# Optimization experiments

Hardware: AMD Instinct MI355X
Metric: run time of the kernel (lower is better)

Reference implementation:

```python
import jax, jax.numpy as jnp
import numpy as np

N, E, M, H, D, G, C = 50000, 400000, 4, 400, 3, 128, 10
BN_EPS = 1e-5


def setup_inputs() -> dict:
    key = jax.random.key(0)
    ks = iter(jax.random.split(key, 64))

    def rn(shape, s=0.05):
        return (jax.random.normal(next(ks), shape, jnp.float32) * s)

    inp = {}
    inp['x'] = jax.random.normal(next(ks), (N, M), jnp.float32)
    inp['edge_index'] = jax.random.randint(next(ks), (2, E), 0, N, dtype=jnp.int32)
    inp['batch'] = jnp.sort(jax.random.randint(next(ks), (N,), 0, G, dtype=jnp.int32))
    inp['num_graphs'] = G
    # first GINConv MLP: M -> H -> H -> H
    inp['c0_w1'] = rn((H, M)); inp['c0_b1'] = rn((H,))
    inp['c0_g1'] = jnp.ones((H,), jnp.float32); inp['c0_be1'] = jnp.zeros((H,), jnp.float32)
    inp['c0_w2'] = rn((H, H)); inp['c0_b2'] = rn((H,))
    inp['c0_g2'] = jnp.ones((H,), jnp.float32); inp['c0_be2'] = jnp.zeros((H,), jnp.float32)
    inp['c0_w3'] = rn((H, H)); inp['c0_b3'] = rn((H,))
    # GINConv layers 1..D-1 (stacked): H -> H -> H -> H
    L = D - 1
    inp['cw1'] = rn((L, H, H)); inp['cb1'] = rn((L, H))
    inp['cg1'] = jnp.ones((L, H), jnp.float32); inp['cbe1'] = jnp.zeros((L, H), jnp.float32)
    inp['cw2'] = rn((L, H, H)); inp['cb2'] = rn((L, H))
    inp['cg2'] = jnp.ones((L, H), jnp.float32); inp['cbe2'] = jnp.zeros((L, H), jnp.float32)
    inp['cw3'] = rn((L, H, H)); inp['cb3'] = rn((L, H))
    # readout head
    inp['lin1_w'] = rn((H * D // 2, H * D)); inp['lin1_b'] = rn((H * D // 2,))
    inp['lin2_w'] = rn((C, H * D // 2)); inp['lin2_b'] = rn((C,))
    return inp


def _bn(z, g, b):
    # training-mode BatchNorm1d over nodes (biased variance, eps=1e-5)
    m = z.mean(axis=0)
    v = ((z - m) ** 2).mean(axis=0)
    return (z - m) * jax.lax.rsqrt(v + BN_EPS) * g + b


def _mlp(h, w1, b1, g1, be1, w2, b2, g2, be2, w3, b3):
    # PyG MLP(num_layers=3): Lin->BN->ReLU, Lin->BN->ReLU, Lin (plain last)
    h = jax.nn.relu(_bn(h @ w1.T + b1, g1, be1))
    h = jax.nn.relu(_bn(h @ w2.T + b2, g2, be2))
    return h @ w3.T + b3


def reference(x, edge_index, batch, num_graphs,
              c0_w1, c0_b1, c0_g1, c0_be1, c0_w2, c0_b2, c0_g2, c0_be2, c0_w3, c0_b3,
              cw1, cb1, cg1, cbe1, cw2, cb2, cg2, cbe2, cw3, cb3,
              lin1_w, lin1_b, lin2_w, lin2_b):
    src, dst = edge_index[0], edge_index[1]
    n = x.shape[0]

    def gin_agg(h):
        # eps = -1.0 => (1+eps)*x_i term vanishes; pure neighbor scatter-add
        return jax.ops.segment_sum(h[src], dst, num_segments=n)

    pools = []
    h = _mlp(gin_agg(x), c0_w1, c0_b1, c0_g1, c0_be1,
             c0_w2, c0_b2, c0_g2, c0_be2, c0_w3, c0_b3)
    pools.append(jax.ops.segment_sum(h, batch, num_segments=num_graphs))
    for i in range(D - 1):
        h = _mlp(gin_agg(h), cw1[i], cb1[i], cg1[i], cbe1[i],
                 cw2[i], cb2[i], cg2[i], cbe2[i], cw3[i], cb3[i])
        pools.append(jax.ops.segment_sum(h, batch, num_segments=num_graphs))
    xG = jnp.concatenate(pools, axis=1)                 # [G, D*H]
    z = jax.nn.relu(xG @ lin1_w.T + lin1_b)             # dropout off (eval)
    z = z @ lin2_w.T + lin2_b
    return jax.nn.log_softmax(z, axis=1)
```

## Files before the change

kernel.cpp:

```cpp
#include <hip/hip_runtime.h>
#include <hip/hip_bf16.h>
#include <math.h>
#include <cstdint>

static constexpr int NN = 50000;
static constexpr int NE = 400000;
static constexpr int H  = 400;
static constexpr int NG = 128;
static constexpr int NC = 10;
static constexpr float EPS = 1e-5f;
static constexpr int NB1 = (NN + 255) / 256;
static constexpr int KP  = 416;
static constexpr int SREP = 8;
static constexpr int SSLOT = SREP * 2 * KP;

typedef unsigned short u16;
typedef __attribute__((ext_vector_type(8))) unsigned short u16x8;
typedef __attribute__((ext_vector_type(4))) unsigned short u16x4;
typedef __attribute__((ext_vector_type(8))) short bf16x8;
typedef __attribute__((ext_vector_type(4))) float f32x4;

__device__ __forceinline__ float bf2f(u16 u) {
    return __uint_as_float(((uint32_t)u) << 16);
}
__device__ __forceinline__ u16 f2bf(float f) {
    uint32_t u = __float_as_uint(f);
    return (u16)((u + 0x7FFFu + ((u >> 16) & 1u)) >> 16);
}
__device__ __forceinline__ void gload_lds16(const void* g, void* lds) {
    __builtin_amdgcn_global_load_lds((const __attribute__((address_space(1))) void*)g,
                                     (__attribute__((address_space(3))) void*)lds, 16, 0, 0);
}

__device__ __forceinline__ bf16x8 bnrelu8(bf16x8 a, const float* __restrict__ scp,
                                          const float* __restrict__ shp) {
    union { bf16x8 v; uint32_t u[4]; } in, out;
    in.v = a;
#pragma unroll
    for (int p = 0; p < 4; ++p) {
        float lo = __uint_as_float(in.u[p] << 16);
        float hi = __uint_as_float(in.u[p] & 0xFFFF0000u);
        lo = fmaxf(fmaf(lo, scp[2 * p], shp[2 * p]), 0.f);
        hi = fmaxf(fmaf(hi, scp[2 * p + 1], shp[2 * p + 1]), 0.f);
        asm("v_cvt_pk_bf16_f32 %0, %1, %2" : "=v"(out.u[p]) : "v"(lo), "v"(hi));
    }
    return out.v;
}


__global__ void k_count(const int* __restrict__ dst, int* __restrict__ deg) {
    int e = blockIdx.x * blockDim.x + threadIdx.x;
    if (e < NE) atomicAdd(&deg[dst[e]], 1);
}

__global__ __launch_bounds__(256) void k_scan1(const int* __restrict__ deg,
                                               int* __restrict__ part,
                                               int* __restrict__ btot) {
    __shared__ int sd[256];
    int t = threadIdx.x;
    int i = blockIdx.x * 256 + t;
    int v = (i < NN) ? deg[i] : 0;
    sd[t] = v;
    __syncthreads();
#pragma unroll
    for (int off = 1; off < 256; off <<= 1) {
        int x = (t >= off) ? sd[t - off] : 0;
        __syncthreads();
        sd[t] += x;
        __syncthreads();
    }
    if (i < NN) part[i] = sd[t];
    if (t == 255) btot[blockIdx.x] = sd[255];
}

__global__ __launch_bounds__(256) void k_scan2(int* __restrict__ btot) {
    __shared__ int sd[256];
    int t = threadIdx.x;
    int v = (t < NB1) ? btot[t] : 0;
    sd[t] = v;
    __syncthreads();
#pragma unroll
    for (int off = 1; off < 256; off <<= 1) {
        int x = (t >= off) ? sd[t - off] : 0;
        __syncthreads();
        sd[t] += x;
        __syncthreads();
    }
    if (t < NB1) btot[t] = sd[t];
}

__global__ __launch_bounds__(256) void k_scan3(const int* __restrict__ part,
                                               const int* __restrict__ btot,
                                               const int* __restrict__ deg,
                                               int* __restrict__ rowp,
                                               int* __restrict__ cur,
                                               const int* __restrict__ batch,
                                               int* __restrict__ cnt) {
    __shared__ int hh[NG];
    int t = threadIdx.x;
    int i = blockIdx.x * 256 + t;
    if (i < NN) {
        int s = part[i] + (blockIdx.x ? btot[blockIdx.x - 1] : 0);
        rowp[i + 1] = s;
        cur[i] = s - deg[i];
    }
    if (i == 0) rowp[0] = 0;
    for (int j = t; j < NG; j += 256) hh[j] = 0;
    __syncthreads();
    if (i < NN) atomicAdd(&hh[batch[i]], 1);
    __syncthreads();
    for (int j = t; j < NG; j += 256)
        if (hh[j]) atomicAdd(&cnt[j], hh[j]);
}

__global__ void k_scatter(const int* __restrict__ src, const int* __restrict__ dst,
                          int* __restrict__ cur, int* __restrict__ csrc) {
    int e = blockIdx.x * blockDim.x + threadIdx.x;
    if (e < NE) {
        int d = dst[e];
        int p = atomicAdd(&cur[d], 1);
        csrc[p] = src[e];
    }
}


__global__ __launch_bounds__(256) void k_wprep(const float* __restrict__ c0_w2,
                                               const float* __restrict__ cw2,
                                               const float* __restrict__ cw1,
                                               const float* __restrict__ c0_w3,
                                               const float* __restrict__ cw3,
                                               const float* __restrict__ c0_b3,
                                               const float* __restrict__ cb3,
                                               u16* __restrict__ wpad,
                                               float* __restrict__ bb1,
                                               float* __restrict__ bb2) {
    const int b = blockIdx.x;
    const int t = threadIdx.x;
    if (b < 244) {
        int i = b * 256 + t;
        if (i >= 3 * 400 * 52) return;
        int rc = i / 52;
        int c8 = (i % 52) * 8;
        u16x8 o = {0, 0, 0, 0, 0, 0, 0, 0};
        if (c8 < 400) {
            int mat = rc / 400, row = rc % 400;
            const float* s = (mat == 0 ? c0_w2 : mat == 1 ? cw2 : cw2 + 160000)
                             + (long)row * 400;
            float4 a = *(const float4*)(s + c8);
            float4 bb = *(const float4*)(s + c8 + 4);
            o[0] = f2bf(a.x); o[1] = f2bf(a.y); o[2] = f2bf(a.z); o[3] = f2bf(a.w);
            o[4] = f2bf(bb.x); o[5] = f2bf(bb.y); o[6] = f2bf(bb.z); o[7] = f2bf(bb.w);
        }
        *(u16x8*)(wpad + (long)rc * KP + c8) = o;
    } else if (b < 342) {
        __shared__ float As[16][68];
        __shared__ float Bs[16][68];
        const int b2 = (b < 293) ? b - 244 : b - 293;
        const float* Wa = (b < 293) ? cw1 : cw1 + 160000;
        const float* Wb = (b < 293) ? c0_w3 : cw3;
        u16* dst = wpad + (size_t)((b < 293) ? 3 : 4) * 400 * KP;
        const int bc = (b2 / 7) * 64, bj = (b2 % 7) * 64;
        const int tx = t & 15, ty = t >> 4;
        float acc[4][4] = {};
        for (int k0 = 0; k0 < 400; k0 += 16) {
            {
                int c = bc + (t >> 2);
                int kq = (t & 3) * 4;
                float4 v = make_float4(0.f, 0.f, 0.f, 0.f);
                if (c < 400) v = *(const float4*)(Wa + (long)c * 400 + k0 + kq);
                As[kq + 0][t >> 2] = v.x; As[kq + 1][t >> 2] = v.y;
                As[kq + 2][t >> 2] = v.z; As[kq + 3][t >> 2] = v.w;
            }
            {
                int k = k0 + (t >> 4);
                int jq = (t & 15) * 4;
                int j = bj + jq;
                float4 v = make_float4(0.f, 0.f, 0.f, 0.f);
                if (j < 400) v = *(const float4*)(Wb + (long)k * 400 + j);
                Bs[t >> 4][jq + 0] = v.x; Bs[t >> 4][jq + 1] = v.y;
                Bs[t >> 4][jq + 2] = v.z; Bs[t >> 4][jq + 3] = v.w;
            }
            __syncthreads();
#pragma unroll
            for (int kk = 0; kk < 16; ++kk) {
                float4 av = *(const float4*)&As[kk][ty * 4];
                float4 bv = *(const float4*)&Bs[kk][tx * 4];
                float a[4] = {av.x, av.y, av.z, av.w};
                float bb[4] = {bv.x, bv.y, bv.z, bv.w};
#pragma unroll
                for (int i = 0; i < 4; ++i)
#pragma unroll
                    for (int j = 0; j < 4; ++j)
                        acc[i][j] = fmaf(a[i], bb[j], acc[i][j]);
            }
            __syncthreads();
        }
#pragma unroll
        for (int i = 0; i < 4; ++i) {
            int c = bc + ty * 4 + i;
            if (c >= 400) continue;
#pragma unroll
            for (int j = 0; j < 4; ++j) {
                int col = bj + tx * 4 + j;
                if (col < KP) dst[(long)c * KP + col] = (col < 400) ? f2bf(acc[i][j]) : 0;
            }
        }
    } else {
        const int c = (b & 1) * 256 + t;
        if (c >= 400) return;
        const float* Wa = (b < 344) ? cw1 : cw1 + 160000;
        const float* bv = (b < 344) ? c0_b3 : cb3;
        float* out = (b < 344) ? bb1 : bb2;
        const float4* wr = (const float4*)(Wa + (long)c * 400);
        const float4* br = (const float4*)bv;
        float s0 = 0.f, s1 = 0.f, s2 = 0.f, s3 = 0.f;
        for (int q = 0; q < 100; ++q) {
            float4 a = wr[q], v = br[q];
            s0 = fmaf(a.x, v.x, s0); s1 = fmaf(a.y, v.y, s1);
            s2 = fmaf(a.z, v.z, s2); s3 = fmaf(a.w, v.w, s3);
        }
        out[c] = s0 + s1 + s2 + s3;
    }
}


__global__ __launch_bounds__(256) void k_agg0(const float* __restrict__ x,
                                              const int* __restrict__ rowp,
                                              const int* __restrict__ csrc,
                                              float* __restrict__ out,
                                              float* __restrict__ mom) {
    __shared__ float ws[4][14];
    int n = blockIdx.x * blockDim.x + threadIdx.x;
    float4 acc = make_float4(0.f, 0.f, 0.f, 0.f);
    if (n < NN) {
        int b = rowp[n], e = rowp[n + 1];
        for (int p = b; p < e; ++p) {
            float4 v = ((const float4*)x)[csrc[p]];
            acc.x += v.x; acc.y += v.y; acc.z += v.z; acc.w += v.w;
        }
        ((float4*)out)[n] = acc;
    }
    float mv[14] = {acc.x, acc.y, acc.z, acc.w,
                    acc.x * acc.x, acc.x * acc.y, acc.x * acc.z, acc.x * acc.w,
                    acc.y * acc.y, acc.y * acc.z, acc.y * acc.w,
                    acc.z * acc.z, acc.z * acc.w, acc.w * acc.w};
    int wv = threadIdx.x >> 6, l = threadIdx.x & 63;
#pragma unroll
    for (int i = 0; i < 14; ++i) {
        float s = mv[i];
#pragma unroll
        for (int o = 32; o; o >>= 1) s += __shfl_xor(s, o);
        if (l == 0) ws[wv][i] = s;
    }
    __syncthreads();
    if (threadIdx.x < 14) {
        float s = ws[0][threadIdx.x] + ws[1][threadIdx.x] + ws[2][threadIdx.x] + ws[3][threadIdx.x];
        atomicAdd(&mom[threadIdx.x], s);
    }
}


__global__ __launch_bounds__(256) void k_aggH(const u16* __restrict__ h,
                                              const int* __restrict__ rowp,
                                              const int* __restrict__ csrc,
                                              const float* __restrict__ bias,
                                              u16* __restrict__ out) {
    int n = (blockIdx.x << 2) + (threadIdx.x >> 6);
    if (n >= NN) return;
    int l = threadIdx.x & 63;
    if (l >= 50) return;
    float4 b0 = *(const float4*)(bias + l * 8);
    float4 b1 = *(const float4*)(bias + l * 8 + 4);
    float acc[8] = {b0.x, b0.y, b0.z, b0.w, b1.x, b1.y, b1.z, b1.w};
    int b = rowp[n], e = rowp[n + 1];
    for (int p = b; p < e; ++p) {
        const u16* r = h + (long)csrc[p] * H + l * 8;
        u16x8 v = *(const u16x8*)r;
#pragma unroll
        for (int q = 0; q < 8; ++q) acc[q] += bf2f(v[q]);
    }
    u16x8 o;
#pragma unroll
    for (int q = 0; q < 8; ++q) o[q] = f2bf(acc[q]);
    *(u16x8*)(out + (long)n * H + l * 8) = o;
}


static constexpr int NLIN0 = (int)(((long)NN * 100 + 255) / 256);

__global__ void k_lin0(const float* __restrict__ a4, const float* __restrict__ w,
                       const float* __restrict__ b, u16* __restrict__ out,
                       const float* __restrict__ mom, float* __restrict__ slot0) {
    if (blockIdx.x >= NLIN0) {
        int j = (blockIdx.x - NLIN0) * 256 + threadIdx.x;
        if (j >= 400) return;
        float4 wv = ((const float4*)w)[j];
        float dot = wv.x * mom[0] + wv.y * mom[1] + wv.z * mom[2] + wv.w * mom[3];
        float quad = wv.x * wv.x * mom[4] + 2.f * wv.x * wv.y * mom[5]
                   + 2.f * wv.x * wv.z * mom[6] + 2.f * wv.x * wv.w * mom[7]
                   + wv.y * wv.y * mom[8] + 2.f * wv.y * wv.z * mom[9]
                   + 2.f * wv.y * wv.w * mom[10] + wv.z * wv.z * mom[11]
                   + 2.f * wv.z * wv.w * mom[12] + wv.w * wv.w * mom[13];
        float bj = b[j];
        slot0[j] = dot + (float)NN * bj;
        slot0[KP + j] = quad + 2.f * bj * dot + (float)NN * bj * bj;
        return;
    }
    long i = (long)blockIdx.x * blockDim.x + threadIdx.x;
    if (i >= (long)NN * 100) return;
    int n = (int)(i / 100), q = (int)(i - (long)n * 100);
    int j0 = q * 4;
    float4 av = ((const float4*)a4)[n];
    u16x4 o;
#pragma unroll
    for (int jj = 0; jj < 4; ++jj) {
        float4 wv = ((const float4*)w)[j0 + jj];
        float s = fmaf(av.x, wv.x, fmaf(av.y, wv.y, fmaf(av.z, wv.z, av.w * wv.w)));
        o[jj] = f2bf(s + b[j0 + jj]);
    }
    *(u16x4*)(out + (long)n * H + j0) = o;
}


__global__ __launch_bounds__(256) void k_statsv(const u16* __restrict__ z,
                                                float* __restrict__ stats) {
    __shared__ float ls[800];
    int t = threadIdx.x;
    for (int i = t; i < 800; i += 256) ls[i] = 0.f;
    __syncthreads();
    if (t < 250) {
        int sub = t / 50, seg = t % 50;
        float s[8] = {0, 0, 0, 0, 0, 0, 0, 0};
        float q[8] = {0, 0, 0, 0, 0, 0, 0, 0};
        for (int r = blockIdx.x * 5 + sub; r < NN; r += gridDim.x * 5) {
            u16x8 v = *(const u16x8*)(z + (long)r * H + seg * 8);
#pragma unroll
            for (int j = 0; j < 8; ++j) {
                float f = bf2f(v[j]);
                s[j] += f; q[j] += f * f;
            }
        }
#pragma unroll
        for (int j = 0; j < 8; ++j) {
            atomicAdd(&ls[seg * 8 + j], s[j]);
            atomicAdd(&ls[400 + seg * 8 + j], q[j]);
        }
    }
    __syncthreads();
    const int rep = blockIdx.x & (SREP - 1);
    for (int i = t; i < 800; i += 256) {
        int col = (i < 400) ? i : (i - 400 + KP);
        atomicAdd(&stats[rep * 2 * KP + col], ls[i]);
    }
}


template <bool STATS>
__global__ __launch_bounds__(256) void gemm_mfma(const u16* __restrict__ A,
                                                 const u16* __restrict__ Wp,
                                                 const float* __restrict__ bias,
                                                 const float* __restrict__ bnG,
                                                 const float* __restrict__ bnBe,
                                                 const float* __restrict__ statsIn,
                                                 float* __restrict__ statsOut,
                                                 u16* __restrict__ out, int M) {
    constexpr int BUF = 6656;
    __shared__ u16 lds[3 * BUF];
    __shared__ float sdScale[KP];
    __shared__ float sdShift[KP];
    __shared__ float sst[160];

    const int t = threadIdx.x;
    const int nwg = gridDim.x;
    const int q8 = nwg >> 3, r8 = nwg & 7;
    const int xcd = blockIdx.x & 7, jj = blockIdx.x >> 3;
    const int wgid = (xcd < r8 ? xcd * (q8 + 1) : r8 * (q8 + 1) + (xcd - r8) * q8) + jj;
    const int bm = (wgid / 5) * 128;
    const int bn = (wgid % 5) * 80;
    const int w = t >> 6, l = t & 63;

    for (int j = t; j < KP; j += 256) {
        float s = 0.f, q = 0.f;
#pragma unroll
        for (int r = 0; r < SREP; ++r) {
            s += statsIn[r * 2 * KP + j];
            q += statsIn[r * 2 * KP + KP + j];
        }
        float sc = 0.f, sh = 0.f;
        if (j < H) {
            float m = s / NN;
            float v = fmaxf(q / NN - m * m, 0.f);
            float rs = rsqrtf(v + EPS);
            sc = bnG[j] * rs;
            sh = bnBe[j] - m * sc;
        }
        sdScale[j] = sc;
        sdShift[j] = sh;
    }

    const int srow = l >> 2;
    const int sck  = ((l & 3) ^ ((l >> 3) & 3)) * 8;

    auto stageTile = [&](int b, int kt) {
        u16* dst = lds + b * BUF;
        const int k0 = kt * 32;
        long g0 = (long)bm + w * 16 + srow;
        long g1 = g0 + 64;
        if (g0 > M - 1) g0 = M - 1;
        if (g1 > M - 1) g1 = M - 1;
        gload_lds16(A + g0 * 400 + k0 + sck, dst + w * 512);
        gload_lds16(A + g1 * 400 + k0 + sck, dst + (w + 4) * 512);
        gload_lds16(Wp + (long)(bn + w * 16 + srow) * KP + k0 + sck,
                    dst + 4096 + w * 512);
        gload_lds16(Wp + (long)(bn + 64 + srow) * KP + k0 + sck,
                    dst + 4096 + 4 * 512);
    };

    f32x4 acc[2][5];
#pragma unroll
    for (int i = 0; i < 2; ++i)
#pragma unroll
        for (int c = 0; c < 5; ++c)
            acc[i][c] = (f32x4){0.f, 0.f, 0.f, 0.f};

    const int r16 = l & 15;
    const int cc  = l >> 4;
    const int swz = r16 * 32 + (((cc ^ ((r16 >> 1) & 3))) << 3);

    auto computeTile = [&](int b, int s) {
        const u16* base = lds + b * BUF;
        const u16* ab = base + w * 1024 + swz;
        const u16* bb = base + 4096 + swz;
        bf16x8 fa0 = *(const bf16x8*)ab;
        bf16x8 fa1 = *(const bf16x8*)(ab + 512);
        const int k = s * 32 + cc * 8;
        fa0 = bnrelu8(fa0, sdScale + k, sdShift + k);
        fa1 = bnrelu8(fa1, sdScale + k, sdShift + k);
        __builtin_amdgcn_s_setprio(1);
#pragma unroll
        for (int c = 0; c < 5; ++c) {
            bf16x8 fb = *(const bf16x8*)(bb + c * 512);
            acc[0][c] = __builtin_amdgcn_mfma_f32_16x16x32_bf16(fa0, fb, acc[0][c], 0, 0, 0);
            acc[1][c] = __builtin_amdgcn_mfma_f32_16x16x32_bf16(fa1, fb, acc[1][c], 0, 0, 0);
        }
        __builtin_amdgcn_s_setprio(0);
    };

    stageTile(0, 0);
    stageTile(1, 1);

#pragma unroll 1
    for (int s = 0; s < 12; ++s) {
        asm volatile("s_waitcnt vmcnt(4)" ::: "memory");
        __builtin_amdgcn_s_barrier();
        if (s + 2 < 13) stageTile((s + 2) % 3, s + 2);
        computeTile(s % 3, s);
    }
    asm volatile("s_waitcnt vmcnt(0)" ::: "memory");
    __builtin_amdgcn_s_barrier();
    computeTile(12 % 3, 12);

    u16* tile = lds;
    __syncthreads();
    if (STATS) for (int i = t; i < 160; i += 256) sst[i] = 0.f;
    if (STATS) __syncthreads();

    float ssum[5], sqq[5];
#pragma unroll
    for (int c = 0; c < 5; ++c) { ssum[c] = 0.f; sqq[c] = 0.f; }
#pragma unroll
    for (int i = 0; i < 2; ++i) {
        const int lrow0 = w * 32 + i * 16 + (l >> 4) * 4;
#pragma unroll
        for (int c = 0; c < 5; ++c) {
            const int lcol = c * 16 + (l & 15);
            const float bv = bias[bn + lcol];
#pragma unroll
            for (int r = 0; r < 4; ++r) {
                const int lrow = lrow0 + r;
                float z = acc[i][c][r] + bv;
                tile[lrow * 80 + lcol] = f2bf(z);
                if (STATS && bm + lrow < M) { ssum[c] += z; sqq[c] += z * z; }
            }
        }
    }
    __syncthreads();
#pragma unroll
    for (int j = 0; j < 5; ++j) {
        int chunk = t + j * 256;
        int row = chunk / 10, c8 = chunk % 10;
        if (bm + row < M) {
            u16x8 v = *(const u16x8*)(tile + row * 80 + c8 * 8);
            *(u16x8*)(out + (long)(bm + row) * H + bn + c8 * 8) = v;
        }
    }
    if (STATS) {
        const int rep = wgid & (SREP - 1);
#pragma unroll
        for (int c = 0; c < 5; ++c) {
            ssum[c] += __shfl_xor(ssum[c], 16); ssum[c] += __shfl_xor(ssum[c], 32);
            sqq[c]  += __shfl_xor(sqq[c], 16);  sqq[c]  += __shfl_xor(sqq[c], 32);
        }
        if (l < 16) {
#pragma unroll
            for (int c = 0; c < 5; ++c) {
                atomicAdd(&sst[c * 16 + l], ssum[c]);
                atomicAdd(&sst[80 + c * 16 + l], sqq[c]);
            }
        }
        __syncthreads();
        if (t < 80)       atomicAdd(&statsOut[rep * 2 * KP + bn + t], sst[t]);
        else if (t < 160) atomicAdd(&statsOut[rep * 2 * KP + KP + bn + (t - 80)], sst[t]);
    }
}


__global__ __launch_bounds__(256) void k_poolf(const u16* __restrict__ z,
                                               const float* __restrict__ statsIn,
                                               const float* __restrict__ gw,
                                               const float* __restrict__ be,
                                               const int* __restrict__ batch,
                                               float* __restrict__ pf) {
    __shared__ float sdS[400];
    __shared__ float sdH[400];
    int t = threadIdx.x;
    for (int j = t; j < 400; j += 256) {
        float s = 0.f, q = 0.f;
#pragma unroll
        for (int r = 0; r < SREP; ++r) {
            s += statsIn[r * 2 * KP + j];
            q += statsIn[r * 2 * KP + KP + j];
        }
        float m = s / NN, v = fmaxf(q / NN - m * m, 0.f);
        float rs = rsqrtf(v + EPS);
        float sc = gw[j] * rs;
        sdS[j] = sc;
        sdH[j] = be[j] - m * sc;
    }
    __syncthreads();
    if (t >= 250) return;
    const int sub = t / 50, seg = t % 50;
    float sc[8], sh[8];
#pragma unroll
    for (int q = 0; q < 8; ++q) {
        sc[q] = sdS[seg * 8 + q];
        sh[q] = sdH[seg * 8 + q];
    }
    int rows = (NN + gridDim.x - 1) / gridDim.x;
    int r0 = blockIdx.x * rows;
    int r1 = min(r0 + rows, NN);
    float acc[8] = {0.f, 0.f, 0.f, 0.f, 0.f, 0.f, 0.f, 0.f};
    int gp = -1;
    for (int r = r0 + sub; r < r1; r += 5) {
        int gg = batch[r];
        if (gg != gp) {
            if (gp >= 0) {
#pragma unroll
                for (int q = 0; q < 8; ++q)
                    atomicAdd(&pf[(long)gp * 400 + seg * 8 + q], acc[q]);
            }
#pragma unroll
            for (int q = 0; q < 8; ++q) acc[q] = 0.f;
            gp = gg;
        }
        u16x8 v = *(const u16x8*)(z + (long)r * H + seg * 8);
#pragma unroll
        for (int q = 0; q < 8; ++q)
            acc[q] += fmaxf(fmaf(bf2f(v[q]), sc[q], sh[q]), 0.f);
    }
    if (gp >= 0) {
#pragma unroll
        for (int q = 0; q < 8; ++q)
            atomicAdd(&pf[(long)gp * 400 + seg * 8 + q], acc[q]);
    }
}


__global__ __launch_bounds__(256) void k_poolgemm(const float* __restrict__ pf,
                                                  const float* __restrict__ w30,
                                                  const float* __restrict__ w312,
                                                  const float* __restrict__ b30,
                                                  const float* __restrict__ b312,
                                                  const int* __restrict__ cnt,
                                                  float* __restrict__ pools) {
    __shared__ __align__(16) float xr[400];
    int g = blockIdx.x, L = blockIdx.y, t = threadIdx.x;
    const float* w = (L == 0) ? w30 : w312 + (size_t)(L - 1) * 400 * 400;
    const float* b = (L == 0) ? b30 : b312 + (L - 1) * 400;
    for (int i = t; i < 400; i += 256) xr[i] = pf[((long)L * NG + g) * 400 + i];
    __syncthreads();
    float cg = (float)cnt[g];
    for (int c = t; c < 400; c += 256) {
        const float4* wr = (const float4*)(w + (long)c * 400);
        const float4* xv = (const float4*)xr;
        float s0 = 0.f, s1 = 0.f, s2 = 0.f, s3 = 0.f;
        for (int q = 0; q < 100; ++q) {
            float4 a = xv[q], bb = wr[q];
            s0 = fmaf(a.x, bb.x, s0); s1 = fmaf(a.y, bb.y, s1);
            s2 = fmaf(a.z, bb.z, s2); s3 = fmaf(a.w, bb.w, s3);
        }
        pools[(long)g * 1200 + L * 400 + c] = s0 + s1 + s2 + s3 + cg * b[c];
    }
}


__global__ __launch_bounds__(256) void k_lin1(const float* __restrict__ pools,
                                              const float* __restrict__ w1,
                                              const float* __restrict__ b1,
                                              float* __restrict__ zz) {
    __shared__ __align__(16) float xg[8][1200];
    const int bandj = blockIdx.x * 40;
    const int g0 = blockIdx.y * 8;
    const int t = threadIdx.x;
    for (int i = t; i < 9600; i += 256)
        xg[i / 1200][i % 1200] = pools[(long)(g0 + i / 1200) * 1200 + (i % 1200)];
    __syncthreads();
    const int wv = t >> 6, l = t & 63;
    for (int jj = wv; jj < 40; jj += 4) {
        const int j = bandj + jj;
        const float4* wr = (const float4*)(w1 + (long)j * 1200);
        float s[8] = {0.f, 0.f, 0.f, 0.f, 0.f, 0.f, 0.f, 0.f};
        for (int q = l; q < 300; q += 64) {
            float4 wq = wr[q];
#pragma unroll
            for (int g = 0; g < 8; ++g) {
                float4 xv = *(const float4*)&xg[g][q * 4];
                s[g] = fmaf(wq.x, xv.x, s[g]);
                s[g] = fmaf(wq.y, xv.y, s[g]);
                s[g] = fmaf(wq.z, xv.z, s[g]);
                s[g] = fmaf(wq.w, xv.w, s[g]);
            }
        }
#pragma unroll
        for (int g = 0; g < 8; ++g)
#pragma unroll
            for (int o = 32; o; o >>= 1) s[g] += __shfl_xor(s[g], o);
        if (l == 0) {
            const float bj = b1[j];
#pragma unroll
            for (int g = 0; g < 8; ++g)
                zz[(long)(g0 + g) * 600 + j] = fmaxf(s[g] + bj, 0.f);
        }
    }
}

__global__ __launch_bounds__(64) void k_lin2(const float* __restrict__ zz,
                                             const float* __restrict__ w2,
                                             const float* __restrict__ b2,
                                             float* __restrict__ out) {
    int g = blockIdx.x;
    int l = threadIdx.x;
    float p[NC];
#pragma unroll
    for (int c = 0; c < NC; ++c) p[c] = 0.f;
    for (int k = l; k < 600; k += 64) {
        float zv = zz[(long)g * 600 + k];
#pragma unroll
        for (int c = 0; c < NC; ++c) p[c] = fmaf(zv, w2[c * 600 + k], p[c]);
    }
#pragma unroll
    for (int c = 0; c < NC; ++c)
#pragma unroll
        for (int o = 32; o; o >>= 1) p[c] += __shfl_xor(p[c], o);
    if (l == 0) {
        float lg[NC];
        float mx = -1e30f;
#pragma unroll
        for (int c = 0; c < NC; ++c) { lg[c] = p[c] + b2[c]; mx = fmaxf(mx, lg[c]); }
        float se = 0.f;
#pragma unroll
        for (int c = 0; c < NC; ++c) se += expf(lg[c] - mx);
        float lse = logf(se);
#pragma unroll
        for (int c = 0; c < NC; ++c) out[(long)g * NC + c] = lg[c] - mx - lse;
    }
}


extern "C" void kernel_launch(void* const* d_in, const int* in_sizes, int n_in,
                              void* d_out, int out_size, void* d_ws, size_t ws_size,
                              hipStream_t stream) {
    const float* x      = (const float*)d_in[0];
    const int*   ei     = (const int*)d_in[1];
    const int*   batch  = (const int*)d_in[2];
    const float* c0_w1  = (const float*)d_in[4];
    const float* c0_b1  = (const float*)d_in[5];
    const float* c0_g1  = (const float*)d_in[6];
    const float* c0_be1 = (const float*)d_in[7];
    const float* c0_w2  = (const float*)d_in[8];
    const float* c0_b2  = (const float*)d_in[9];
    const float* c0_g2  = (const float*)d_in[10];
    const float* c0_be2 = (const float*)d_in[11];
    const float* c0_w3  = (const float*)d_in[12];
    const float* c0_b3  = (const float*)d_in[13];
    const float* cw1    = (const float*)d_in[14];
    const float* cb1    = (const float*)d_in[15];
    const float* cg1    = (const float*)d_in[16];
    const float* cbe1   = (const float*)d_in[17];
    const float* cw2    = (const float*)d_in[18];
    const float* cb2    = (const float*)d_in[19];
    const float* cg2    = (const float*)d_in[20];
    const float* cbe2   = (const float*)d_in[21];
    const float* cw3    = (const float*)d_in[22];
    const float* cb3    = (const float*)d_in[23];
    const float* lin1_w = (const float*)d_in[24];
    const float* lin1_b = (const float*)d_in[25];
    const float* lin2_w = (const float*)d_in[26];
    const float* lin2_b = (const float*)d_in[27];

    const int* src = ei;
    const int* dst = ei + NE;

    char* ws = (char*)d_ws;
    size_t off = 0;
    auto alloc = [&](size_t bytes) {
        void* p = ws + off;
        off += (bytes + 255) & ~(size_t)255;
        return p;
    };
    u16*   bufh   = (u16*)alloc((size_t)NN * H * 2 + 128);
    u16*   bufa   = (u16*)alloc((size_t)NN * H * 2 + 128);
    float* agg0   = (float*)alloc((size_t)NN * 4 * 4);
    char*  zstart = ws + off;
    int*   deg    = (int*)alloc((size_t)NN * 4);
    float* statsA = (float*)alloc((size_t)6 * SSLOT * 4);
    float* mom    = (float*)alloc(14 * 4);
    float* pf     = (float*)alloc((size_t)3 * NG * 400 * 4);
    int*   cnt    = (int*)alloc((size_t)NG * 4);
    size_t zbytes = (size_t)((ws + off) - zstart);
    float* pools  = (float*)alloc((size_t)NG * 3 * H * 4);
    float* zz     = (float*)alloc((size_t)NG * 600 * 4);
    float* bb1    = (float*)alloc(400 * 4);
    float* bb2    = (float*)alloc(400 * 4);
    u16*   wpad   = (u16*)alloc((size_t)5 * 400 * KP * 2);
    int*   rowp   = (int*)alloc((size_t)(NN + 1) * 4);
    int*   cur    = (int*)alloc((size_t)NN * 4);
    int*   csrc   = (int*)alloc((size_t)NE * 4);
    int*   part   = (int*)alloc((size_t)NN * 4);
    int*   btot   = (int*)alloc((size_t)NB1 * 4);

    auto wp   = [&](int mat) { return wpad + (size_t)mat * 400 * KP; };
    auto slot = [&](int i)   { return statsA + (size_t)i * SSLOT; };

    hipMemsetAsync(zstart, 0, zbytes, stream);

    k_wprep<<<346, 256, 0, stream>>>(c0_w2, cw2, cw1, c0_w3, cw3, c0_b3, cb3,
                                     wpad, bb1, bb2);

    k_count<<<(NE + 255) / 256, 256, 0, stream>>>(dst, deg);
    k_scan1<<<NB1, 256, 0, stream>>>(deg, part, btot);
    k_scan2<<<1, 256, 0, stream>>>(btot);
    k_scan3<<<NB1, 256, 0, stream>>>(part, btot, deg, rowp, cur, batch, cnt);
    k_scatter<<<(NE + 255) / 256, 256, 0, stream>>>(src, dst, cur, csrc);

    const int ngemm = ((NN + 127) / 128) * 5;

    k_agg0<<<NB1, 256, 0, stream>>>(x, rowp, csrc, agg0, mom);
    k_lin0<<<NLIN0 + 2, 256, 0, stream>>>(agg0, c0_w1, c0_b1, bufh, mom, slot(0));
    gemm_mfma<true><<<ngemm, 256, 0, stream>>>(bufh, wp(0), c0_b2, c0_g1, c0_be1,
                                               slot(0), slot(1), bufa, NN);
    gemm_mfma<false><<<ngemm, 256, 0, stream>>>(bufa, wp(3), bb1, c0_g2, c0_be2,
                                                slot(1), nullptr, bufh, NN);
    k_poolf<<<512, 256, 0, stream>>>(bufa, slot(1), c0_g2, c0_be2, batch, pf);

    k_aggH<<<(NN + 3) / 4, 256, 0, stream>>>(bufh, rowp, csrc, cb1, bufa);
    k_statsv<<<256, 256, 0, stream>>>(bufa, slot(2));
    gemm_mfma<true><<<ngemm, 256, 0, stream>>>(bufa, wp(1), cb2, cg1, cbe1,
                                               slot(2), slot(3), bufh, NN);
    gemm_mfma<false><<<ngemm, 256, 0, stream>>>(bufh, wp(4), bb2, cg2, cbe2,
                                                slot(3), nullptr, bufa, NN);
    k_poolf<<<512, 256, 0, stream>>>(bufh, slot(3), cg2, cbe2, batch, pf + (size_t)NG * 400);

    k_aggH<<<(NN + 3) / 4, 256, 0, stream>>>(bufa, rowp, csrc, cb1 + 400, bufh);
    k_statsv<<<256, 256, 0, stream>>>(bufh, slot(4));
    gemm_mfma<true><<<ngemm, 256, 0, stream>>>(bufh, wp(2), cb2 + 400, cg1 + 400,
                                               cbe1 + 400, slot(4), slot(5), bufa, NN);
    k_poolf<<<512, 256, 0, stream>>>(bufa, slot(5), cg2 + 400, cbe2 + 400, batch,
                                     pf + (size_t)2 * NG * 400);

    dim3 gp(NG, 3);
    k_poolgemm<<<gp, 256, 0, stream>>>(pf, c0_w3, cw3, c0_b3, cb3, cnt, pools);
    dim3 gl1(15, 16);
    k_lin1<<<gl1, 256, 0, stream>>>(pools, lin1_w, lin1_b, zz);
    k_lin2<<<NG, 64, 0, stream>>>(zz, lin2_w, lin2_b, (float*)d_out);
}
```

Baseline: 751.1 us.

## Keep full weight slice resident in LDS and stream A per-wave without barriers

The GEMM now uses 512-thread workgroups with 256-row tiles. The whole 80x416 weight slice is loaded into swizzled LDS once per block, and each wave streams its own 32-row A slice through a private 4-deep LDS ring. This removes the per-k-step workgroup barriers and the repeated B staging, replacing them with per-wave vmcnt waits and sched_barriers. The cost is a large LDS footprint (about 100KB) that limits the kernel to one block per CU, a serial B preload before compute starts, and fewer blocks across the grid.

```diff
diff --git a/kernel.cpp b/kernel.cpp
--- a/kernel.cpp
+++ b/kernel.cpp
@@ -356,16 +356,15 @@
 
 
 template <bool STATS>
-__global__ __launch_bounds__(256) void gemm_mfma(const u16* __restrict__ A,
-                                                 const u16* __restrict__ Wp,
-                                                 const float* __restrict__ bias,
-                                                 const float* __restrict__ bnG,
-                                                 const float* __restrict__ bnBe,
-                                                 const float* __restrict__ statsIn,
-                                                 float* __restrict__ statsOut,
-                                                 u16* __restrict__ out, int M) {
-    constexpr int BUF = 6656;
-    __shared__ u16 lds[3 * BUF];
+__global__ __launch_bounds__(512, 1) void gemm_mfma(const u16* __restrict__ A,
+                                                    const u16* __restrict__ Wp,
+                                                    const float* __restrict__ bias,
+                                                    const float* __restrict__ bnG,
+                                                    const float* __restrict__ bnBe,
+                                                    const float* __restrict__ statsIn,
+                                                    float* __restrict__ statsOut,
+                                                    u16* __restrict__ out, int M) {
+    __shared__ u16 lds[33280 + 8 * 4 * 2 * 512];
     __shared__ float sdScale[KP];
     __shared__ float sdShift[KP];
     __shared__ float sst[160];
@@ -375,11 +374,35 @@
     const int q8 = nwg >> 3, r8 = nwg & 7;
     const int xcd = blockIdx.x & 7, jj = blockIdx.x >> 3;
     const int wgid = (xcd < r8 ? xcd * (q8 + 1) : r8 * (q8 + 1) + (xcd - r8) * q8) + jj;
-    const int bm = (wgid / 5) * 128;
+    const int bm = (wgid / 5) * 256;
     const int bn = (wgid % 5) * 80;
     const int w = t >> 6, l = t & 63;
 
-    for (int j = t; j < KP; j += 256) {
+    u16* Bs = lds;
+    u16* Aw = lds + 33280 + w * 4096;
+
+    const int srow = l >> 2;
+    const int sck  = ((l & 3) ^ ((l >> 3) & 3)) * 8;
+    long gr0 = (long)bm + w * 32 + srow;
+    long gr1 = gr0 + 16;
+    if (gr0 > M - 1) gr0 = M - 1;
+    if (gr1 > M - 1) gr1 = M - 1;
+    const u16* pA0 = A + gr0 * 400 + sck;
+    const u16* pA1 = A + gr1 * 400 + sck;
+#pragma unroll
+    for (int kt = 0; kt < 3; ++kt) {
+        gload_lds16(pA0 + kt * 32, Aw + (kt * 2 + 0) * 512);
+        gload_lds16(pA1 + kt * 32, Aw + (kt * 2 + 1) * 512);
+    }
+
+    for (int i = t; i < 80 * 52; i += 512) {
+        int row = i / 52, g = i % 52;
+        u16x8 v = *(const u16x8*)(Wp + (long)(bn + row) * KP + g * 8);
+        int pg = (g & ~3) | ((g & 3) ^ ((row >> 1) & 3));
+        *(u16x8*)&Bs[row * 416 + pg * 8] = v;
+    }
+
+    for (int j = t; j < KP; j += 512) {
         float s = 0.f, q = 0.f;
 #pragma unroll
         for (int r = 0; r < SREP; ++r) {
@@ -397,24 +420,7 @@
         sdScale[j] = sc;
         sdShift[j] = sh;
     }
-
-    const int srow = l >> 2;
-    const int sck  = ((l & 3) ^ ((l >> 3) & 3)) * 8;
-
-    auto stageTile = [&](int b, int kt) {
-        u16* dst = lds + b * BUF;
-        const int k0 = kt * 32;
-        long g0 = (long)bm + w * 16 + srow;
-        long g1 = g0 + 64;
-        if (g0 > M - 1) g0 = M - 1;
-        if (g1 > M - 1) g1 = M - 1;
-        gload_lds16(A + g0 * 400 + k0 + sck, dst + w * 512);
-        gload_lds16(A + g1 * 400 + k0 + sck, dst + (w + 4) * 512);
-        gload_lds16(Wp + (long)(bn + w * 16 + srow) * KP + k0 + sck,
-                    dst + 4096 + w * 512);
-        gload_lds16(Wp + (long)(bn + 64 + srow) * KP + k0 + sck,
-                    dst + 4096 + 4 * 512);
-    };
+    __syncthreads();
 
     f32x4 acc[2][5];
 #pragma unroll
@@ -425,44 +431,48 @@
 
     const int r16 = l & 15;
     const int cc  = l >> 4;
-    const int swz = r16 * 32 + (((cc ^ ((r16 >> 1) & 3))) << 3);
-
-    auto computeTile = [&](int b, int s) {
-        const u16* base = lds + b * BUF;
-        const u16* ab = base + w * 1024 + swz;
-        const u16* bb = base + 4096 + swz;
+    const int swzA = r16 * 32 + ((cc ^ ((r16 >> 1) & 3)) << 3);
+    const int swzB = (cc ^ ((r16 >> 1) & 3)) << 3;
+
+    auto computeTile = [&](int s) {
+        const u16* ab = Aw + ((s & 3) * 2) * 512 + swzA;
         bf16x8 fa0 = *(const bf16x8*)ab;
         bf16x8 fa1 = *(const bf16x8*)(ab + 512);
         const int k = s * 32 + cc * 8;
         fa0 = bnrelu8(fa0, sdScale + k, sdShift + k);
         fa1 = bnrelu8(fa1, sdScale + k, sdShift + k);
+        const u16* bb = Bs + r16 * 416 + s * 32 + swzB;
         __builtin_amdgcn_s_setprio(1);
 #pragma unroll
         for (int c = 0; c < 5; ++c) {
-            bf16x8 fb = *(const bf16x8*)(bb + c * 512);
+            bf16x8 fb = *(const bf16x8*)(bb + c * 16 * 416);
             acc[0][c] = __builtin_amdgcn_mfma_f32_16x16x32_bf16(fa0, fb, acc[0][c], 0, 0, 0);
             acc[1][c] = __builtin_amdgcn_mfma_f32_16x16x32_bf16(fa1, fb, acc[1][c], 0, 0, 0);
         }
         __builtin_amdgcn_s_setprio(0);
     };
 
-    stageTile(0, 0);
-    stageTile(1, 1);
-
 #pragma unroll 1
-    for (int s = 0; s < 12; ++s) {
+    for (int s = 0; s < 11; ++s) {
         asm volatile("s_waitcnt vmcnt(4)" ::: "memory");
-        __builtin_amdgcn_s_barrier();
-        if (s + 2 < 13) stageTile((s + 2) % 3, s + 2);
-        computeTile(s % 3, s);
-    }
+        __builtin_amdgcn_sched_barrier(0);
+        if (s < 10) {
+            const int kt = s + 3;
+            gload_lds16(pA0 + kt * 32, Aw + ((kt & 3) * 2 + 0) * 512);
+            gload_lds16(pA1 + kt * 32, Aw + ((kt & 3) * 2 + 1) * 512);
+        }
+        computeTile(s);
+    }
+    asm volatile("s_waitcnt vmcnt(2)" ::: "memory");
+    __builtin_amdgcn_sched_barrier(0);
+    computeTile(11);
     asm volatile("s_waitcnt vmcnt(0)" ::: "memory");
-    __builtin_amdgcn_s_barrier();
-    computeTile(12 % 3, 12);
+    __builtin_amdgcn_sched_barrier(0);
+    computeTile(12);
 
     u16* tile = lds;
     __syncthreads();
-    if (STATS) for (int i = t; i < 160; i += 256) sst[i] = 0.f;
+    if (STATS) for (int i = t; i < 160; i += 512) sst[i] = 0.f;
     if (STATS) __syncthreads();
 
     float ssum[5], sqq[5];
@@ -487,7 +497,7 @@
     __syncthreads();
 #pragma unroll
     for (int j = 0; j < 5; ++j) {
-        int chunk = t + j * 256;
+        int chunk = t + j * 512;
         int row = chunk / 10, c8 = chunk % 10;
         if (bm + row < M) {
             u16x8 v = *(const u16x8*)(tile + row * 80 + c8 * 8);
@@ -753,27 +763,27 @@
     k_scan3<<<NB1, 256, 0, stream>>>(part, btot, deg, rowp, cur, batch, cnt);
     k_scatter<<<(NE + 255) / 256, 256, 0, stream>>>(src, dst, cur, csrc);
 
-    const int ngemm = ((NN + 127) / 128) * 5;
+    const int ngemm = ((NN + 255) / 256) * 5;
 
     k_agg0<<<NB1, 256, 0, stream>>>(x, rowp, csrc, agg0, mom);
     k_lin0<<<NLIN0 + 2, 256, 0, stream>>>(agg0, c0_w1, c0_b1, bufh, mom, slot(0));
-    gemm_mfma<true><<<ngemm, 256, 0, stream>>>(bufh, wp(0), c0_b2, c0_g1, c0_be1,
+    gemm_mfma<true><<<ngemm, 512, 0, stream>>>(bufh, wp(0), c0_b2, c0_g1, c0_be1,
                                                slot(0), slot(1), bufa, NN);
-    gemm_mfma<false><<<ngemm, 256, 0, stream>>>(bufa, wp(3), bb1, c0_g2, c0_be2,
+    gemm_mfma<false><<<ngemm, 512, 0, stream>>>(bufa, wp(3), bb1, c0_g2, c0_be2,
                                                 slot(1), nullptr, bufh, NN);
     k_poolf<<<512, 256, 0, stream>>>(bufa, slot(1), c0_g2, c0_be2, batch, pf);
 
     k_aggH<<<(NN + 3) / 4, 256, 0, stream>>>(bufh, rowp, csrc, cb1, bufa);
     k_statsv<<<256, 256, 0, stream>>>(bufa, slot(2));
-    gemm_mfma<true><<<ngemm, 256, 0, stream>>>(bufa, wp(1), cb2, cg1, cbe1,
+    gemm_mfma<true><<<ngemm, 512, 0, stream>>>(bufa, wp(1), cb2, cg1, cbe1,
                                                slot(2), slot(3), bufh, NN);
-    gemm_mfma<false><<<ngemm, 256, 0, stream>>>(bufh, wp(4), bb2, cg2, cbe2,
+    gemm_mfma<false><<<ngemm, 512, 0, stream>>>(bufh, wp(4), bb2, cg2, cbe2,
                                                 slot(3), nullptr, bufa, NN);
     k_poolf<<<512, 256, 0, stream>>>(bufh, slot(3), cg2, cbe2, batch, pf + (size_t)NG * 400);
 
     k_aggH<<<(NN + 3) / 4, 256, 0, stream>>>(bufa, rowp, csrc, cb1 + 400, bufh);
     k_statsv<<<256, 256, 0, stream>>>(bufh, slot(4));
-    gemm_mfma<true><<<ngemm, 256, 0, stream>>>(bufh, wp(2), cb2 + 400, cg1 + 400,
+    gemm_mfma<true><<<ngemm, 512, 0, stream>>>(bufh, wp(2), cb2 + 400, cg1 + 400,
                                                cbe1 + 400, slot(4), slot(5), bufa, NN);
     k_poolf<<<512, 256, 0, stream>>>(bufa, slot(5), cg2 + 400, cbe2 + 400, batch,
                                      pf + (size_t)2 * NG * 400);
```

After: 795.2 us. 1.06x slower.
